# Optimization experiments

Hardware: AMD Instinct MI355X
Metric: run time of the kernel (lower is better)

Reference implementation:

```python
import jax, jax.numpy as jnp
import numpy as np
from functools import partial

T, B, IN, H, OUT = 512, 64, 512, 1024, 512


def _qrnn_layer(x, W, b):
    """One QRNN layer (window=1, fo-pool). x: (T,B,D) -> (T,B,H)."""
    g = jnp.einsum('tbd,dh->tbh', x, W) + b        # (T,B,3H)
    z, f, o = jnp.split(g, 3, axis=-1)
    z = jnp.tanh(z)
    f = jax.nn.sigmoid(f)
    o = jax.nn.sigmoid(o)

    def step(c, zf):
        z_t, f_t = zf
        c = f_t * c + (1.0 - f_t) * z_t            # fo-pool recurrence
        return c, c

    c0 = jnp.zeros((x.shape[1], W.shape[1] // 3), x.dtype)
    _, cs = jax.lax.scan(step, c0, (z, f))         # cs: (T,B,H)
    return o * cs


def setup_inputs() -> dict:
    key = jax.random.key(0)
    ks = jax.random.split(key, 5)
    scale = lambda fan_in: 1.0 / np.sqrt(fan_in)
    return {
        'x':   jax.random.normal(ks[0], (T, B, IN), jnp.float32),
        'W0':  jax.random.normal(ks[1], (IN, 3 * H), jnp.float32) * scale(IN),
        'b0':  jnp.zeros((3 * H,), jnp.float32),
        'W1':  jax.random.normal(ks[2], (H, 3 * H), jnp.float32) * scale(H),
        'b1':  jnp.zeros((3 * H,), jnp.float32),
        'Wfc': jax.random.normal(ks[3], (H, OUT), jnp.float32) * scale(H),
        'bfc': jnp.zeros((OUT,), jnp.float32),
    }


def reference(x, W0, b0, W1, b1, Wfc, bfc):
    h = _qrnn_layer(x, W0, b0)                     # layer 0: (T,B,H)
    h = _qrnn_layer(h, W1, b1)                     # layer 1: (T,B,H)
    out = jnp.einsum('tbh,ho->tbo', h, Wfc) + bfc  # fc over all timesteps
    return out
```

## Files before the change

### kernel.cpp

```cpp
#include <hip/hip_runtime.h>
#include <hip/hip_bf16.h>


#define QT 512
#define QB 64
#define QIN 512
#define QH 1024
#define QOUT 512
#define QM (QT * QB)
#define SEG 32
#define SL (QT / SEG)

typedef unsigned short ushort_t;
typedef __attribute__((ext_vector_type(8))) short bf16x8;
typedef __attribute__((ext_vector_type(4))) float f32x4;

__device__ __forceinline__ float blo(unsigned int u) {
    union { unsigned int i; float f; } v;
    v.i = u << 16;
    return v.f;
}

__device__ __forceinline__ float bhi(unsigned int u) {
    union { unsigned int i; float f; } v;
    v.i = u & 0xffff0000u;
    return v.f;
}

__device__ __forceinline__ ushort_t f2bf(float f) {
    union { float f; unsigned int i; } v;
    v.f = f;
    unsigned int r = v.i + 0x7fffu + ((v.i >> 16) & 1u);
    return (ushort_t)(r >> 16);
}

__device__ __forceinline__ void glds16(const ushort_t* g, ushort_t* l) {
    __builtin_amdgcn_global_load_lds(
        (const __attribute__((address_space(1))) void*)g,
        (__attribute__((address_space(3))) void*)l, 16, 0, 0);
}

__global__ __launch_bounds__(256) void cvt_bf16(const float* __restrict__ src,
                                                ushort_t* __restrict__ dst) {
    const int i = blockIdx.x * 256 + threadIdx.x;
    float4 v = ((const float4*)src)[i];
    ushort4 o;
    o.x = f2bf(v.x); o.y = f2bf(v.y); o.z = f2bf(v.z); o.w = f2bf(v.w);
    ((ushort4*)dst)[i] = o;
}

__global__ __launch_bounds__(256) void transpose_cvt(
    const float* __restrict__ W, ushort_t* __restrict__ WT, int K, int N) {
    __shared__ float t[32][33];
    const int tx = threadIdx.x & 31, ty = threadIdx.x >> 5;
    const int n0 = blockIdx.x * 32, k0 = blockIdx.y * 32;
#pragma unroll
    for (int i = 0; i < 4; ++i)
        t[ty + 8 * i][tx] = W[(size_t)(k0 + ty + 8 * i) * N + n0 + tx];
    __syncthreads();
#pragma unroll
    for (int i = 0; i < 4; ++i)
        WT[(size_t)(n0 + ty + 8 * i) * K + k0 + tx] = f2bf(t[tx][ty + 8 * i]);
}

template <int MODE, int K>
__global__ __launch_bounds__(512, 2) void gemm256(
    const ushort_t* __restrict__ A, const ushort_t* __restrict__ BT,
    const float* __restrict__ bias, void* __restrict__ out,
    int c0, int CW) {
    constexpr int NT = K / 32;
    __shared__ ushort_t As[4 * 8192];
    __shared__ ushort_t Bs[4 * 8192];

    const int tid = threadIdx.x;
    const int lane = tid & 63;
    const int w = tid >> 6;
    const int wr = w >> 2, wc = w & 3;

    const int gx = gridDim.x;
    const int nwg = gx * gridDim.y;
    int flat = blockIdx.y * gx + blockIdx.x;
    flat = (flat & 7) * (nwg >> 3) + (flat >> 3);
    const int by = flat / gx;
    const int bx = flat - by * gx;
    const int m0 = by * 256;

    int nW, nOut, outstride, gate = 0;
    if (MODE == 0) {
        const int per = CW >> 8;
        gate = bx / per;
        const int nloc = (bx - gate * per) * 256;
        nW = gate * QH + c0 + nloc;
        nOut = gate * CW + nloc;
        outstride = 3 * CW;
    } else {
        nW = bx * 256;
        nOut = nW;
        outstride = QOUT;
    }

    size_t aoff[2], boff[2];
    int ldso[2];
#pragma unroll
    for (int j = 0; j < 2; ++j) {
        const int c = w * 128 + j * 64 + lane;
        const int r = c >> 2;
        const int gs = (c & 3) ^ ((r >> 1) & 3);
        aoff[j] = (size_t)(m0 + r) * K + gs * 8;
        boff[j] = (size_t)(nW + r) * K + gs * 8;
        ldso[j] = w * 1024 + j * 512;
    }

    const int fl = lane & 15, fq = lane >> 4;
    const int laneoff = fl * 32 + ((fq ^ ((fl >> 1) & 3)) << 3);

    f32x4 acc[8][4];
#pragma unroll
    for (int i = 0; i < 8; ++i)
#pragma unroll
        for (int j = 0; j < 4; ++j) acc[i][j] = {0.f, 0.f, 0.f, 0.f};

#pragma unroll
    for (int t = 0; t < 3; ++t) {
        const int slot = t * 8192;
#pragma unroll
        for (int j = 0; j < 2; ++j)
            glds16(A + aoff[j] + t * 32, &As[slot + ldso[j]]);
#pragma unroll
        for (int j = 0; j < 2; ++j)
            glds16(BT + boff[j] + t * 32, &Bs[slot + ldso[j]]);
    }
    asm volatile("s_waitcnt vmcnt(8)" ::: "memory");
    __builtin_amdgcn_s_barrier();

    for (int kt = 0; kt < NT; ++kt) {
        const int slot = (kt & 3) * 8192;
        const int sa = slot + wr * 4096 + laneoff;
        const int sb = slot + wc * 2048 + laneoff;
        const bool pf = (kt + 3 < NT);
        const int pslot = ((kt + 3) & 3) * 8192;
        const size_t kb = (size_t)(kt + 3) * 32;

        bf16x8 a0[4], a1[4], bv[4];
#pragma unroll
        for (int i = 0; i < 4; ++i) a0[i] = *(const bf16x8*)&As[sa + i * 512];
#pragma unroll
        for (int j = 0; j < 4; ++j) bv[j] = *(const bf16x8*)&Bs[sb + j * 512];
        if (pf) {
#pragma unroll
            for (int j = 0; j < 2; ++j)
                glds16(A + aoff[j] + kb, &As[pslot + ldso[j]]);
        }
        __builtin_amdgcn_sched_barrier(0);
        __builtin_amdgcn_s_barrier();
        asm volatile("s_waitcnt lgkmcnt(0)" ::: "memory");
        __builtin_amdgcn_sched_barrier(0);
        __builtin_amdgcn_s_setprio(1);
#pragma unroll
        for (int i = 0; i < 4; ++i)
#pragma unroll
            for (int j = 0; j < 4; ++j)
                acc[i][j] = __builtin_amdgcn_mfma_f32_16x16x32_bf16(
                    a0[i], bv[j], acc[i][j], 0, 0, 0);
        __builtin_amdgcn_s_setprio(0);
        __builtin_amdgcn_sched_barrier(0);
        __builtin_amdgcn_s_barrier();
#pragma unroll
        for (int i = 0; i < 4; ++i)
            a1[i] = *(const bf16x8*)&As[sa + (4 + i) * 512];
        if (pf) {
#pragma unroll
            for (int j = 0; j < 2; ++j)
                glds16(BT + boff[j] + kb, &Bs[pslot + ldso[j]]);
        }
        __builtin_amdgcn_sched_barrier(0);
        __builtin_amdgcn_s_barrier();
        asm volatile("s_waitcnt lgkmcnt(0)" ::: "memory");
        __builtin_amdgcn_sched_barrier(0);
        __builtin_amdgcn_s_setprio(1);
#pragma unroll
        for (int i = 0; i < 4; ++i)
#pragma unroll
            for (int j = 0; j < 4; ++j)
                acc[4 + i][j] = __builtin_amdgcn_mfma_f32_16x16x32_bf16(
                    a1[i], bv[j], acc[4 + i][j], 0, 0, 0);
        __builtin_amdgcn_s_setprio(0);
        if (kt < NT - 3)
            asm volatile("s_waitcnt vmcnt(8)" ::: "memory");
        else if (kt == NT - 3)
            asm volatile("s_waitcnt vmcnt(4)" ::: "memory");
        else if (kt == NT - 2)
            asm volatile("s_waitcnt vmcnt(0)" ::: "memory");
        __builtin_amdgcn_sched_barrier(0);
        if (kt < NT - 1) __builtin_amdgcn_s_barrier();
    }

    const float ak = (gate == 0) ? 2.8853900817779268f : -1.4426950408889634f;
    const float aa = (gate == 0) ? -2.f : 1.f;
    const float ad = (gate == 0) ? 1.f : 0.f;

    float bvv[4];
#pragma unroll
    for (int j = 0; j < 4; ++j) bvv[j] = bias[nW + wc * 64 + j * 16 + fl];
#pragma unroll
    for (int i = 0; i < 8; ++i) {
#pragma unroll
        for (int r = 0; r < 4; ++r) {
            const int row = m0 + wr * 128 + i * 16 + fq * 4 + r;
#pragma unroll
            for (int j = 0; j < 4; ++j) {
                const int col = nOut + wc * 64 + j * 16 + fl;
                float v = acc[i][j][r] + bvv[j];
                if (MODE == 0) {
                    v = aa * __builtin_amdgcn_rcpf(
                                 1.f + __builtin_amdgcn_exp2f(ak * v)) +
                        ad;
                    ((ushort_t*)out)[(size_t)row * outstride + col] = f2bf(v);
                } else {
                    ((float*)out)[(size_t)row * outstride + col] = v;
                }
            }
        }
    }
}


__global__ __launch_bounds__(256) void scan_p1(const ushort_t* __restrict__ g,
                                               float* __restrict__ Aseg,
                                               float* __restrict__ Bseg,
                                               int CW) {
    const int idx4 = blockIdx.x * 256 + threadIdx.x;
    const int cw4 = CW >> 2;
    const int hh = (idx4 % cw4) << 2;
    const int sb = idx4 / cw4;
    const int b = sb % QB;
    const int s = sb / QB;
    const ushort_t* gp = g + ((size_t)(s * SL * QB + b) * 3) * CW + hh;
    const size_t grow = (size_t)QB * 3 * CW;
    uint2 zu[SL], fu[SL];
#pragma unroll
    for (int t = 0; t < SL; ++t) {
        zu[t] = *(const uint2*)gp;
        fu[t] = *(const uint2*)(gp + CW);
        gp += grow;
    }
    float4 A = {1.f, 1.f, 1.f, 1.f}, Bc = {0.f, 0.f, 0.f, 0.f};
#pragma unroll
    for (int t = 0; t < SL; ++t) {
        const float f0 = blo(fu[t].x), f1 = bhi(fu[t].x);
        const float f2 = blo(fu[t].y), f3 = bhi(fu[t].y);
        Bc.x = f0 * Bc.x + (1.f - f0) * blo(zu[t].x);
        Bc.y = f1 * Bc.y + (1.f - f1) * bhi(zu[t].x);
        Bc.z = f2 * Bc.z + (1.f - f2) * blo(zu[t].y);
        Bc.w = f3 * Bc.w + (1.f - f3) * bhi(zu[t].y);
        A.x *= f0; A.y *= f1; A.z *= f2; A.w *= f3;
    }
    const size_t oidx = (size_t)sb * CW + hh;
    *(float4*)&Aseg[oidx] = A;
    *(float4*)&Bseg[oidx] = Bc;
}

__global__ __launch_bounds__(256) void scan_p3(const ushort_t* __restrict__ g,
                                               const float* __restrict__ Aseg,
                                               const float* __restrict__ Bseg,
                                               ushort_t* __restrict__ h,
                                               int c0, int CW) {
    const int idx4 = blockIdx.x * 256 + threadIdx.x;
    const int cw4 = CW >> 2;
    const int hh = (idx4 % cw4) << 2;
    const int sb = idx4 / cw4;
    const int b = sb % QB;
    const int s = sb / QB;
    const ushort_t* gp = g + ((size_t)(s * SL * QB + b) * 3) * CW + hh;
    ushort_t* hp = h + (size_t)(s * SL * QB + b) * QH + c0 + hh;
    const size_t grow = (size_t)QB * 3 * CW;
    const size_t hrow = (size_t)QB * QH;
    uint2 zu[SL], fu[SL], ou[SL];
#pragma unroll
    for (int t = 0; t < SL; ++t) {
        zu[t] = *(const uint2*)gp;
        fu[t] = *(const uint2*)(gp + CW);
        ou[t] = *(const uint2*)(gp + 2 * CW);
        gp += grow;
    }
    float4 c = {0.f, 0.f, 0.f, 0.f};
    const size_t stride = (size_t)QB * CW;
    const size_t colo = (size_t)b * CW + hh;
    int sp = 0;
    while (sp + 8 <= s) {
        float4 Av[8], Bv[8];
#pragma unroll
        for (int q = 0; q < 8; ++q) {
            const size_t o = (size_t)(sp + q) * stride + colo;
            Av[q] = *(const float4*)&Aseg[o];
            Bv[q] = *(const float4*)&Bseg[o];
        }
#pragma unroll
        for (int q = 0; q < 8; ++q) {
            c.x = Av[q].x * c.x + Bv[q].x;
            c.y = Av[q].y * c.y + Bv[q].y;
            c.z = Av[q].z * c.z + Bv[q].z;
            c.w = Av[q].w * c.w + Bv[q].w;
        }
        sp += 8;
    }
    if (sp < s) {
        float4 Av[8], Bv[8];
#pragma unroll
        for (int q = 0; q < 8; ++q) {
            const int si = (sp + q < SEG) ? sp + q : SEG - 1;
            const size_t o = (size_t)si * stride + colo;
            Av[q] = *(const float4*)&Aseg[o];
            Bv[q] = *(const float4*)&Bseg[o];
        }
#pragma unroll
        for (int q = 0; q < 8; ++q) {
            if (sp + q < s) {
                c.x = Av[q].x * c.x + Bv[q].x;
                c.y = Av[q].y * c.y + Bv[q].y;
                c.z = Av[q].z * c.z + Bv[q].z;
                c.w = Av[q].w * c.w + Bv[q].w;
            }
        }
    }
#pragma unroll
    for (int t = 0; t < SL; ++t) {
        const float f0 = blo(fu[t].x), f1 = bhi(fu[t].x);
        const float f2 = blo(fu[t].y), f3 = bhi(fu[t].y);
        c.x = f0 * c.x + (1.f - f0) * blo(zu[t].x);
        c.y = f1 * c.y + (1.f - f1) * bhi(zu[t].x);
        c.z = f2 * c.z + (1.f - f2) * blo(zu[t].y);
        c.w = f3 * c.w + (1.f - f3) * bhi(zu[t].y);
        ushort4 hv;
        hv.x = f2bf(blo(ou[t].x) * c.x);
        hv.y = f2bf(bhi(ou[t].x) * c.y);
        hv.z = f2bf(blo(ou[t].y) * c.z);
        hv.w = f2bf(bhi(ou[t].y) * c.w);
        *(ushort4*)hp = hv;
        hp += hrow;
    }
}

extern "C" void kernel_launch(void* const* d_in, const int* in_sizes, int n_in,
                              void* d_out, int out_size, void* d_ws,
                              size_t ws_size, hipStream_t stream) {
    const float* x   = (const float*)d_in[0];
    const float* W0  = (const float*)d_in[1];
    const float* b0  = (const float*)d_in[2];
    const float* W1  = (const float*)d_in[3];
    const float* b1  = (const float*)d_in[4];
    const float* Wfc = (const float*)d_in[5];
    const float* bfc = (const float*)d_in[6];
    float* out = (float*)d_out;

    char* p = (char*)d_ws;
    ushort_t* h0   = (ushort_t*)p;  p += (size_t)QM * QH * 2;
    ushort_t* h1   = (ushort_t*)p;
    ushort_t* x_bf = (ushort_t*)p;  p += (size_t)QM * QH * 2;
    ushort_t* W0T  = (ushort_t*)p;  p += (size_t)3 * QH * QIN * 2;
    ushort_t* W1T  = (ushort_t*)p;  p += (size_t)3 * QH * QH * 2;
    ushort_t* WfcT = (ushort_t*)p;  p += (size_t)QOUT * QH * 2;
    const size_t base = (size_t)(p - (char*)d_ws);

    int CW = QH;
    while (CW > 256 &&
           base + 2 * (size_t)QB * CW * SEG * 4 + (size_t)QM * 3 * CW * 2 >
               ws_size)
        CW >>= 1;
    const int nch = QH / CW;

    float* Aseg   = (float*)p;  p += (size_t)QB * CW * SEG * 4;
    float* Bseg   = (float*)p;  p += (size_t)QB * CW * SEG * 4;
    ushort_t* g   = (ushort_t*)p;

    dim3 blk(256);
    dim3 blk5(512);

    cvt_bf16<<<dim3(QM * QIN / 1024), blk, 0, stream>>>(x, x_bf);
    transpose_cvt<<<dim3(3 * QH / 32, QIN / 32), blk, 0, stream>>>(
        W0, W0T, QIN, 3 * QH);
    transpose_cvt<<<dim3(3 * QH / 32, QH / 32), blk, 0, stream>>>(
        W1, W1T, QH, 3 * QH);
    transpose_cvt<<<dim3(QOUT / 32, QH / 32), blk, 0, stream>>>(
        Wfc, WfcT, QH, QOUT);

    const dim3 ggrid(3 * (CW >> 8), QM / 256);
    const dim3 p13grid(SEG * QB * CW / 1024);

    for (int ci = 0; ci < nch; ++ci) {
        gemm256<0, QIN><<<ggrid, blk5, 0, stream>>>(x_bf, W0T, b0, g,
                                                    ci * CW, CW);
        scan_p1<<<p13grid, blk, 0, stream>>>(g, Aseg, Bseg, CW);
        scan_p3<<<p13grid, blk, 0, stream>>>(g, Aseg, Bseg, h0, ci * CW, CW);
    }
    for (int ci = 0; ci < nch; ++ci) {
        gemm256<0, QH><<<ggrid, blk5, 0, stream>>>(h0, W1T, b1, g,
                                                   ci * CW, CW);
        scan_p1<<<p13grid, blk, 0, stream>>>(g, Aseg, Bseg, CW);
        scan_p3<<<p13grid, blk, 0, stream>>>(g, Aseg, Bseg, h1, ci * CW, CW);
    }
    gemm256<1, QH><<<dim3(QOUT / 256, QM / 256), blk5, 0, stream>>>(
        h1, WfcT, bfc, out, 0, 0);
}
```

Before: 675.4 us.

## Shrink GEMM tile to 128x256 with 4 waves and 3-stage LDS pipeline

Restructures the bf16 MFMA GEMM from 256x256 tiles with 8 waves and a 4-deep LDS ring to 128x256 tiles with 4 waves (2x2 wave grid, each wave 64x128) and a 3-stage rotating buffer. B loads per thread double and the second MFMA half now reuses the A fragments against new B fragments. The grid doubles in M and LDS per block shrinks from 128KB to 72KB. The aim is more blocks in flight and better load balance across CUs, at the cost of lower arithmetic intensity per block and a shallower prefetch distance.

```diff
diff --git a/kernel.cpp b/kernel.cpp
--- a/kernel.cpp
+++ b/kernel.cpp
@@ -64,18 +64,18 @@
 }
 
 template <int MODE, int K>
-__global__ __launch_bounds__(512, 2) void gemm256(
+__global__ __launch_bounds__(256, 2) void gemm256(
     const ushort_t* __restrict__ A, const ushort_t* __restrict__ BT,
     const float* __restrict__ bias, void* __restrict__ out,
     int c0, int CW) {
     constexpr int NT = K / 32;
-    __shared__ ushort_t As[4 * 8192];
-    __shared__ ushort_t Bs[4 * 8192];
+    __shared__ ushort_t As[3 * 4096];
+    __shared__ ushort_t Bs[3 * 8192];
 
     const int tid = threadIdx.x;
     const int lane = tid & 63;
     const int w = tid >> 6;
-    const int wr = w >> 2, wc = w & 3;
+    const int wr = w >> 1, wc = w & 1;
 
     const int gx = gridDim.x;
     const int nwg = gx * gridDim.y;
@@ -83,7 +83,7 @@
     flat = (flat & 7) * (nwg >> 3) + (flat >> 3);
     const int by = flat / gx;
     const int bx = flat - by * gx;
-    const int m0 = by * 256;
+    const int m0 = by * 128;
 
     int nW, nOut, outstride, gate = 0;
     if (MODE == 0) {
@@ -99,57 +99,64 @@
         outstride = QOUT;
     }
 
-    size_t aoff[2], boff[2];
-    int ldso[2];
+    size_t aoff[2];
+    int ldsoA[2];
 #pragma unroll
     for (int j = 0; j < 2; ++j) {
         const int c = w * 128 + j * 64 + lane;
         const int r = c >> 2;
         const int gs = (c & 3) ^ ((r >> 1) & 3);
         aoff[j] = (size_t)(m0 + r) * K + gs * 8;
+        ldsoA[j] = w * 1024 + j * 512;
+    }
+    size_t boff[4];
+    int ldsoB[4];
+#pragma unroll
+    for (int j = 0; j < 4; ++j) {
+        const int c = w * 256 + j * 64 + lane;
+        const int r = c >> 2;
+        const int gs = (c & 3) ^ ((r >> 1) & 3);
         boff[j] = (size_t)(nW + r) * K + gs * 8;
-        ldso[j] = w * 1024 + j * 512;
+        ldsoB[j] = w * 2048 + j * 512;
     }
 
     const int fl = lane & 15, fq = lane >> 4;
     const int laneoff = fl * 32 + ((fq ^ ((fl >> 1) & 3)) << 3);
 
-    f32x4 acc[8][4];
-#pragma unroll
-    for (int i = 0; i < 8; ++i)
-#pragma unroll
-        for (int j = 0; j < 4; ++j) acc[i][j] = {0.f, 0.f, 0.f, 0.f};
-
-#pragma unroll
-    for (int t = 0; t < 3; ++t) {
-        const int slot = t * 8192;
+    f32x4 acc[4][8];
+#pragma unroll
+    for (int i = 0; i < 4; ++i)
+#pragma unroll
+        for (int j = 0; j < 8; ++j) acc[i][j] = {0.f, 0.f, 0.f, 0.f};
+
+#pragma unroll
+    for (int t = 0; t < 2; ++t) {
 #pragma unroll
         for (int j = 0; j < 2; ++j)
-            glds16(A + aoff[j] + t * 32, &As[slot + ldso[j]]);
-#pragma unroll
-        for (int j = 0; j < 2; ++j)
-            glds16(BT + boff[j] + t * 32, &Bs[slot + ldso[j]]);
-    }
-    asm volatile("s_waitcnt vmcnt(8)" ::: "memory");
+            glds16(A + aoff[j] + t * 32, &As[t * 4096 + ldsoA[j]]);
+#pragma unroll
+        for (int j = 0; j < 4; ++j)
+            glds16(BT + boff[j] + t * 32, &Bs[t * 8192 + ldsoB[j]]);
+    }
+    asm volatile("s_waitcnt vmcnt(6)" ::: "memory");
     __builtin_amdgcn_s_barrier();
 
+    int cur = 0, stg = 2;
     for (int kt = 0; kt < NT; ++kt) {
-        const int slot = (kt & 3) * 8192;
-        const int sa = slot + wr * 4096 + laneoff;
-        const int sb = slot + wc * 2048 + laneoff;
-        const bool pf = (kt + 3 < NT);
-        const int pslot = ((kt + 3) & 3) * 8192;
-        const size_t kb = (size_t)(kt + 3) * 32;
-
-        bf16x8 a0[4], a1[4], bv[4];
-#pragma unroll
-        for (int i = 0; i < 4; ++i) a0[i] = *(const bf16x8*)&As[sa + i * 512];
-#pragma unroll
-        for (int j = 0; j < 4; ++j) bv[j] = *(const bf16x8*)&Bs[sb + j * 512];
+        const int sA = cur * 4096 + wr * 2048 + laneoff;
+        const int sB = cur * 8192 + wc * 4096 + laneoff;
+        const bool pf = (kt + 2 < NT);
+        const size_t kb = (size_t)(kt + 2) * 32;
+
+        bf16x8 af[4], bv[4], bw[4];
+#pragma unroll
+        for (int i = 0; i < 4; ++i) af[i] = *(const bf16x8*)&As[sA + i * 512];
+#pragma unroll
+        for (int j = 0; j < 4; ++j) bv[j] = *(const bf16x8*)&Bs[sB + j * 512];
         if (pf) {
 #pragma unroll
             for (int j = 0; j < 2; ++j)
-                glds16(A + aoff[j] + kb, &As[pslot + ldso[j]]);
+                glds16(A + aoff[j] + kb, &As[stg * 4096 + ldsoA[j]]);
         }
         __builtin_amdgcn_sched_barrier(0);
         __builtin_amdgcn_s_barrier();
@@ -161,17 +168,17 @@
 #pragma unroll
             for (int j = 0; j < 4; ++j)
                 acc[i][j] = __builtin_amdgcn_mfma_f32_16x16x32_bf16(
-                    a0[i], bv[j], acc[i][j], 0, 0, 0);
+                    af[i], bv[j], acc[i][j], 0, 0, 0);
         __builtin_amdgcn_s_setprio(0);
         __builtin_amdgcn_sched_barrier(0);
         __builtin_amdgcn_s_barrier();
 #pragma unroll
-        for (int i = 0; i < 4; ++i)
-            a1[i] = *(const bf16x8*)&As[sa + (4 + i) * 512];
+        for (int j = 0; j < 4; ++j)
+            bw[j] = *(const bf16x8*)&Bs[sB + (4 + j) * 512];
         if (pf) {
 #pragma unroll
-            for (int j = 0; j < 2; ++j)
-                glds16(BT + boff[j] + kb, &Bs[pslot + ldso[j]]);
+            for (int j = 0; j < 4; ++j)
+                glds16(BT + boff[j] + kb, &Bs[stg * 8192 + ldsoB[j]]);
         }
         __builtin_amdgcn_sched_barrier(0);
         __builtin_amdgcn_s_barrier();
@@ -182,34 +189,34 @@
         for (int i = 0; i < 4; ++i)
 #pragma unroll
             for (int j = 0; j < 4; ++j)
-                acc[4 + i][j] = __builtin_amdgcn_mfma_f32_16x16x32_bf16(
-                    a1[i], bv[j], acc[4 + i][j], 0, 0, 0);
+                acc[i][4 + j] = __builtin_amdgcn_mfma_f32_16x16x32_bf16(
+                    af[i], bw[j], acc[i][4 + j], 0, 0, 0);
         __builtin_amdgcn_s_setprio(0);
-        if (kt < NT - 3)
-            asm volatile("s_waitcnt vmcnt(8)" ::: "memory");
-        else if (kt == NT - 3)
-            asm volatile("s_waitcnt vmcnt(4)" ::: "memory");
+        if (kt < NT - 2)
+            asm volatile("s_waitcnt vmcnt(6)" ::: "memory");
         else if (kt == NT - 2)
             asm volatile("s_waitcnt vmcnt(0)" ::: "memory");
         __builtin_amdgcn_sched_barrier(0);
         if (kt < NT - 1) __builtin_amdgcn_s_barrier();
+        cur = (cur == 2) ? 0 : cur + 1;
+        stg = (stg == 2) ? 0 : stg + 1;
     }
 
     const float ak = (gate == 0) ? 2.8853900817779268f : -1.4426950408889634f;
     const float aa = (gate == 0) ? -2.f : 1.f;
     const float ad = (gate == 0) ? 1.f : 0.f;
 
-    float bvv[4];
-#pragma unroll
-    for (int j = 0; j < 4; ++j) bvv[j] = bias[nW + wc * 64 + j * 16 + fl];
-#pragma unroll
-    for (int i = 0; i < 8; ++i) {
+    float bvv[8];
+#pragma unroll
+    for (int j = 0; j < 8; ++j) bvv[j] = bias[nW + wc * 128 + j * 16 + fl];
+#pragma unroll
+    for (int i = 0; i < 4; ++i) {
 #pragma unroll
         for (int r = 0; r < 4; ++r) {
-            const int row = m0 + wr * 128 + i * 16 + fq * 4 + r;
-#pragma unroll
-            for (int j = 0; j < 4; ++j) {
-                const int col = nOut + wc * 64 + j * 16 + fl;
+            const int row = m0 + wr * 64 + i * 16 + fq * 4 + r;
+#pragma unroll
+            for (int j = 0; j < 8; ++j) {
+                const int col = nOut + wc * 128 + j * 16 + fl;
                 float v = acc[i][j][r] + bvv[j];
                 if (MODE == 0) {
                     v = aa * __builtin_amdgcn_rcpf(
@@ -374,7 +381,6 @@
     ushort_t* g   = (ushort_t*)p;
 
     dim3 blk(256);
-    dim3 blk5(512);
 
     cvt_bf16<<<dim3(QM * QIN / 1024), blk, 0, stream>>>(x, x_bf);
     transpose_cvt<<<dim3(3 * QH / 32, QIN / 32), blk, 0, stream>>>(
@@ -384,21 +390,21 @@
     transpose_cvt<<<dim3(QOUT / 32, QH / 32), blk, 0, stream>>>(
         Wfc, WfcT, QH, QOUT);
 
-    const dim3 ggrid(3 * (CW >> 8), QM / 256);
+    const dim3 ggrid(3 * (CW >> 8), QM / 128);
     const dim3 p13grid(SEG * QB * CW / 1024);
 
     for (int ci = 0; ci < nch; ++ci) {
-        gemm256<0, QIN><<<ggrid, blk5, 0, stream>>>(x_bf, W0T, b0, g,
-                                                    ci * CW, CW);
+        gemm256<0, QIN><<<ggrid, blk, 0, stream>>>(x_bf, W0T, b0, g,
+                                                   ci * CW, CW);
         scan_p1<<<p13grid, blk, 0, stream>>>(g, Aseg, Bseg, CW);
         scan_p3<<<p13grid, blk, 0, stream>>>(g, Aseg, Bseg, h0, ci * CW, CW);
     }
     for (int ci = 0; ci < nch; ++ci) {
-        gemm256<0, QH><<<ggrid, blk5, 0, stream>>>(h0, W1T, b1, g,
-                                                   ci * CW, CW);
+        gemm256<0, QH><<<ggrid, blk, 0, stream>>>(h0, W1T, b1, g,
+                                                  ci * CW, CW);
         scan_p1<<<p13grid, blk, 0, stream>>>(g, Aseg, Bseg, CW);
         scan_p3<<<p13grid, blk, 0, stream>>>(g, Aseg, Bseg, h1, ci * CW, CW);
     }
-    gemm256<1, QH><<<dim3(QOUT / 256, QM / 256), blk5, 0, stream>>>(
+    gemm256<1, QH><<<dim3(QOUT / 256, QM / 128), blk, 0, stream>>>(
         h1, WfcT, bfc, out, 0, 0);
 }
```

Measured after the change: 668.9 us. Within noise of the previous version (-1.0%).
